# Optimization experiments

Measured on AMD Instinct MI355X. Metric: run time of the kernel, lower is better.

The kernel has to match this reference:

```python
import jax, jax.numpy as jnp
import numpy as np

TOKENS = 1024
IN_W = 512
BLOCK = 256
OUT_W = 512
N_BLOCKS = 64
K = 2


def setup_inputs() -> dict:
    key = jax.random.key(0)
    ks = jax.random.split(key, 8)
    u = lambda k, s: jax.random.uniform(k, s, jnp.float32, -1.0, 1.0)
    return {
        "x": jax.random.normal(ks[0], (TOKENS, IN_W), jnp.float32),
        "noise": jax.random.normal(ks[1], (TOKENS, N_BLOCKS), jnp.float32),
        "w1s": u(ks[2], (N_BLOCKS, IN_W, BLOCK)),
        "b1s": u(ks[3], (N_BLOCKS, BLOCK)),
        "w2s": u(ks[4], (N_BLOCKS, BLOCK, OUT_W)),
        "b2s": u(ks[5], (N_BLOCKS, OUT_W)),
        "mixer": jnp.zeros((IN_W, N_BLOCKS), jnp.float32) + 0.01 * jax.random.normal(ks[6], (IN_W, N_BLOCKS), jnp.float32),
        "noise_controller": jnp.zeros((IN_W, N_BLOCKS), jnp.float32) + 0.01 * jax.random.normal(ks[7], (IN_W, N_BLOCKS), jnp.float32),
        "k": K,
    }


def reference(x, noise, w1s, b1s, w2s, b2s, mixer, noise_controller, k):
    # noisy routing logits: mixer_prod + randn * softplus(noise_prod)
    h_x = x @ mixer + noise * jax.nn.softplus(x @ noise_controller)  # [B, E]
    topk_vals, topk_idx = jax.lax.top_k(h_x, k)                       # [B, K]
    scores = jax.nn.softmax(topk_vals, axis=-1)                       # [B, K]
    # per-token expert weight gather (faithful to index_select semantics)
    gw1 = w1s[topk_idx]  # [B, K, I, H]
    gb1 = b1s[topk_idx]  # [B, K, H]
    gw2 = w2s[topk_idx]  # [B, K, H, O]
    gb2 = b2s[topk_idx]  # [B, K, O]
    v = jax.nn.relu(jnp.einsum('bi,bkih->bkh', x, gw1) + gb1)        # [B, K, H]
    out = jnp.einsum('bkh,bkho->bko', v, gw2) + gb2                   # [B, K, O]
    return jnp.sum(out * scores[..., None], axis=1)                   # [B, O]
```

## Files before the change

kernel.cpp:

```cpp
#include <hip/hip_runtime.h>
#include <math.h>

#define TOKENS    1024
#define IN_W      512
#define BLOCK_H   256
#define OUT_W     512
#define N_EXPERTS 64
#define TOPK      2
#define NSLOTS    (TOKENS * TOPK)
#define LIST_CAP  128
#define T_GRP     12
#define NGRP      4
#define XPAD      520
#define OSPAD     516
#define VPAD      264

__global__ __launch_bounds__(256) void routing_kernel(
    const float* __restrict__ x, const float* __restrict__ noise,
    const float* __restrict__ mixer, const float* __restrict__ noisec,
    float* __restrict__ esc, int* __restrict__ counts, int* __restrict__ lists)
{
    __shared__ float xs[2 * 512];
    __shared__ float pm[2 * 2 * 64];
    __shared__ float pn[2 * 2 * 64];
    const int blk  = blockIdx.x;
    const int tid  = threadIdx.x;
    const int wave = tid >> 6, lane = tid & 63;
    const int tq = wave >> 1;
    const int ih = wave & 1;

    ((float4*)xs)[tid] = ((const float4*)x)[(size_t)blk * 256 + tid];
    __syncthreads();

    float am = 0.f, an = 0.f;
    const float* xp = xs + tq * 512 + ih * 256;
    const float* mp = mixer  + (size_t)(ih * 256) * 64 + lane;
    const float* np = noisec + (size_t)(ih * 256) * 64 + lane;
    #pragma unroll 8
    for (int i = 0; i < 256; ++i) {
        const float xv = xp[i];
        am = fmaf(xv, mp[i * 64], am);
        an = fmaf(xv, np[i * 64], an);
    }
    pm[tq * 128 + ih * 64 + lane] = am;
    pn[tq * 128 + ih * 64 + lane] = an;
    __syncthreads();

    if (tid < 128) {
        const int e = tid & 63, tt = tid >> 6;
        const int t = blk * 2 + tt;
        const float am2 = pm[tt * 128 + e] + pm[tt * 128 + 64 + e];
        const float an2 = pn[tt * 128 + e] + pn[tt * 128 + 64 + e];
        const float sp = fmaxf(an2, 0.f) + log1pf(expf(-fabsf(an2)));
        pm[tt * 128 + e] = am2 + noise[(size_t)t * 64 + e] * sp;
    }
    __syncthreads();

    if (tid < 2) {
        const float* h = pm + tid * 128;
        float b0 = -INFINITY, b1 = -INFINITY;
        int i0 = 0, i1 = 0;
        for (int i = 0; i < N_EXPERTS; ++i) {
            const float v = h[i];
            if (v > b0)      { b1 = b0; i1 = i0; b0 = v; i0 = i; }
            else if (v > b1) { b1 = v; i1 = i; }
        }
        const float z   = expf(b1 - b0);
        const float inv = 1.f / (1.f + z);
        const int t = blk * 2 + tid;
        esc[t * 2 + 0] = inv;
        esc[t * 2 + 1] = z * inv;
        const int p0 = atomicAdd(&counts[i0], 1);
        if (p0 < LIST_CAP) lists[i0 * LIST_CAP + p0] = t * 2 + 0;
        const int p1 = atomicAdd(&counts[i1], 1);
        if (p1 < LIST_CAP) lists[i1 * LIST_CAP + p1] = t * 2 + 1;
    }
}

__global__ __launch_bounds__(1024, 4) void expert_kernel(
    const float* __restrict__ x,
    const float* __restrict__ w1s, const float* __restrict__ b1s,
    const float* __restrict__ w2s, const float* __restrict__ b2s,
    const int* __restrict__ counts, const int* __restrict__ lists,
    const float* __restrict__ esc, float* __restrict__ out)
{
    __shared__ __align__(16) float smem[T_GRP * XPAD];
    __shared__ __align__(16) float vsm[T_GRP * VPAD];
    __shared__ int   slotIds[T_GRP];
    __shared__ float escv[T_GRP];

    const int e  = blockIdx.x;
    const int g  = blockIdx.y;
    const int ne = min(counts[e], LIST_CAP);
    const int tid  = threadIdx.x;
    const int wave = tid >> 6, lane = tid & 63;

    const int cq1  = wave & 3;
    const int tt   = wave >> 2;
    const int c4_1 = cq1 * 16 + (lane & 15);
    const int r1   = lane >> 4;
    const int c4_2 = cq1 * 32 + (lane & 31);
    const int r2   = lane >> 5;
    const int t0   = tt * 3;

    const float4* w1v = (const float4*)(w1s + (size_t)e * IN_W * BLOCK_H);
    const float4* w2v = (const float4*)(w2s + (size_t)e * BLOCK_H * OUT_W);
    const float4* b1v = (const float4*)(b1s + (size_t)e * BLOCK_H);
    const float4* b2v = (const float4*)(b2s + (size_t)e * OUT_W);
    const float4* x4  = (const float4*)x;

    for (int base = g * T_GRP; base < ne; base += NGRP * T_GRP) {
        const int nTok = min(T_GRP, ne - base);
        if (tid < T_GRP) {
            const int s = (tid < nTok) ? lists[e * LIST_CAP + base + tid] : 0;
            slotIds[tid] = s;
            escv[tid]    = esc[s];
        }
        __syncthreads();

        for (int idx = tid; idx < T_GRP * 128; idx += 1024) {
            const int t = idx >> 7, q = idx & 127;
            float4 v = make_float4(0.f, 0.f, 0.f, 0.f);
            if (t < nTok) v = x4[(size_t)(slotIds[t] >> 1) * 128 + q];
            *(float4*)&smem[t * XPAD + q * 4] = v;
        }
        __syncthreads();

        float4 a0 = make_float4(0.f, 0.f, 0.f, 0.f), a1 = a0, a2 = a0;
        {
            const float4* wp = w1v + (size_t)(r1 * 64 + c4_1);
            const float* xb0 = smem + (t0 + 0) * XPAD + r1;
            const float* xb1 = smem + (t0 + 1) * XPAD + r1;
            const float* xb2 = smem + (t0 + 2) * XPAD + r1;
            #pragma unroll 4
            for (int i = 0; i < IN_W; i += 4) {
                const float4 w = wp[(size_t)i * 64];
                const float xv0 = xb0[i], xv1 = xb1[i], xv2 = xb2[i];
                a0.x = fmaf(xv0, w.x, a0.x); a0.y = fmaf(xv0, w.y, a0.y);
                a0.z = fmaf(xv0, w.z, a0.z); a0.w = fmaf(xv0, w.w, a0.w);
                a1.x = fmaf(xv1, w.x, a1.x); a1.y = fmaf(xv1, w.y, a1.y);
                a1.z = fmaf(xv1, w.z, a1.z); a1.w = fmaf(xv1, w.w, a1.w);
                a2.x = fmaf(xv2, w.x, a2.x); a2.y = fmaf(xv2, w.y, a2.y);
                a2.z = fmaf(xv2, w.z, a2.z); a2.w = fmaf(xv2, w.w, a2.w);
            }
        }
        #pragma unroll
        for (int m = 16; m <= 32; m <<= 1) {
            a0.x += __shfl_xor(a0.x, m); a0.y += __shfl_xor(a0.y, m);
            a0.z += __shfl_xor(a0.z, m); a0.w += __shfl_xor(a0.w, m);
            a1.x += __shfl_xor(a1.x, m); a1.y += __shfl_xor(a1.y, m);
            a1.z += __shfl_xor(a1.z, m); a1.w += __shfl_xor(a1.w, m);
            a2.x += __shfl_xor(a2.x, m); a2.y += __shfl_xor(a2.y, m);
            a2.z += __shfl_xor(a2.z, m); a2.w += __shfl_xor(a2.w, m);
        }
        if (lane < 16) {
            const float4 bb = b1v[c4_1];
            float4 r;
            r.x = fmaxf(a0.x + bb.x, 0.f); r.y = fmaxf(a0.y + bb.y, 0.f);
            r.z = fmaxf(a0.z + bb.z, 0.f); r.w = fmaxf(a0.w + bb.w, 0.f);
            *(float4*)&vsm[(t0 + 0) * VPAD + c4_1 * 4] = r;
            r.x = fmaxf(a1.x + bb.x, 0.f); r.y = fmaxf(a1.y + bb.y, 0.f);
            r.z = fmaxf(a1.z + bb.z, 0.f); r.w = fmaxf(a1.w + bb.w, 0.f);
            *(float4*)&vsm[(t0 + 1) * VPAD + c4_1 * 4] = r;
            r.x = fmaxf(a2.x + bb.x, 0.f); r.y = fmaxf(a2.y + bb.y, 0.f);
            r.z = fmaxf(a2.z + bb.z, 0.f); r.w = fmaxf(a2.w + bb.w, 0.f);
            *(float4*)&vsm[(t0 + 2) * VPAD + c4_1 * 4] = r;
        }
        __syncthreads();

        float4 o0 = make_float4(0.f, 0.f, 0.f, 0.f), o1 = o0, o2 = o0;
        {
            const float4* wp2 = w2v + (size_t)(r2 * 128 + c4_2);
            const float* vb0 = vsm + (t0 + 0) * VPAD + r2;
            const float* vb1 = vsm + (t0 + 1) * VPAD + r2;
            const float* vb2 = vsm + (t0 + 2) * VPAD + r2;
            #pragma unroll 4
            for (int h = 0; h < BLOCK_H; h += 2) {
                const float4 w = wp2[(size_t)h * 128];
                const float v0 = vb0[h], v1 = vb1[h], v2 = vb2[h];
                o0.x = fmaf(v0, w.x, o0.x); o0.y = fmaf(v0, w.y, o0.y);
                o0.z = fmaf(v0, w.z, o0.z); o0.w = fmaf(v0, w.w, o0.w);
                o1.x = fmaf(v1, w.x, o1.x); o1.y = fmaf(v1, w.y, o1.y);
                o1.z = fmaf(v1, w.z, o1.z); o1.w = fmaf(v1, w.w, o1.w);
                o2.x = fmaf(v2, w.x, o2.x); o2.y = fmaf(v2, w.y, o2.y);
                o2.z = fmaf(v2, w.z, o2.z); o2.w = fmaf(v2, w.w, o2.w);
            }
        }
        o0.x += __shfl_xor(o0.x, 32); o0.y += __shfl_xor(o0.y, 32);
        o0.z += __shfl_xor(o0.z, 32); o0.w += __shfl_xor(o0.w, 32);
        o1.x += __shfl_xor(o1.x, 32); o1.y += __shfl_xor(o1.y, 32);
        o1.z += __shfl_xor(o1.z, 32); o1.w += __shfl_xor(o1.w, 32);
        o2.x += __shfl_xor(o2.x, 32); o2.y += __shfl_xor(o2.y, 32);
        o2.z += __shfl_xor(o2.z, 32); o2.w += __shfl_xor(o2.w, 32);
        if (lane < 32) {
            *(float4*)&smem[(t0 + 0) * OSPAD + c4_2 * 4] = o0;
            *(float4*)&smem[(t0 + 1) * OSPAD + c4_2 * 4] = o1;
            *(float4*)&smem[(t0 + 2) * OSPAD + c4_2 * 4] = o2;
        }
        __syncthreads();

        for (int idx = tid; idx < T_GRP * 128; idx += 1024) {
            const int t = idx >> 7, q = idx & 127;
            if (t < nTok) {
                const float4 r  = *(const float4*)&smem[t * OSPAD + q * 4];
                const float4 bb = b2v[q];
                const float  sc = escv[t];
                float* o = out + (size_t)(slotIds[t] >> 1) * OUT_W + q * 4;
                atomicAdd(o + 0, (r.x + bb.x) * sc);
                atomicAdd(o + 1, (r.y + bb.y) * sc);
                atomicAdd(o + 2, (r.z + bb.z) * sc);
                atomicAdd(o + 3, (r.w + bb.w) * sc);
            }
        }
        __syncthreads();
    }
}

extern "C" void kernel_launch(void* const* d_in, const int* in_sizes, int n_in,
                              void* d_out, int out_size, void* d_ws, size_t ws_size,
                              hipStream_t stream) {
    const float* x      = (const float*)d_in[0];
    const float* noise  = (const float*)d_in[1];
    const float* w1s    = (const float*)d_in[2];
    const float* b1s    = (const float*)d_in[3];
    const float* w2s    = (const float*)d_in[4];
    const float* b2s    = (const float*)d_in[5];
    const float* mixer  = (const float*)d_in[6];
    const float* noisec = (const float*)d_in[7];
    float* out = (float*)d_out;

    char* ws = (char*)d_ws;
    int*   counts = (int*)ws;                       ws += 256;
    float* esc    = (float*)ws;                     ws += NSLOTS * sizeof(float);
    int*   lists  = (int*)ws;

    hipMemsetAsync(d_out, 0, (size_t)out_size * sizeof(float), stream);
    hipMemsetAsync(counts, 0, 256, stream);

    routing_kernel<<<TOKENS / 2, 256, 0, stream>>>(x, noise, mixer, noisec,
                                                   esc, counts, lists);
    expert_kernel<<<dim3(N_EXPERTS, NGRP), 1024, 0, stream>>>(
        x, w1s, b1s, w2s, b2s, counts, lists, esc, out);
}
```

Baseline: 180.4 us.

## Vectorize LDS activation reads, prefetch weights in registers, retile second GEMM

The first GEMM now gives each lane four consecutive input rows and reads activations from shared memory as float4. Weight rows are double-buffered in registers, so the next 16-row chunk is loaded while the current one is consumed. The second GEMM is retiled so each wave covers 16 output float4 columns for 6 tokens instead of 32 columns for 3 tokens. Each weight load is therefore reused across more tokens, at the cost of more accumulator registers and a two-step shuffle reduction. The larger register footprint under the 1024-thread launch bound could force spills or lower occupancy.

```diff
diff --git a/kernel.cpp b/kernel.cpp
--- a/kernel.cpp
+++ b/kernel.cpp
@@ -95,13 +95,14 @@
     const int tid  = threadIdx.x;
     const int wave = tid >> 6, lane = tid & 63;
 
-    const int cq1  = wave & 3;
-    const int tt   = wave >> 2;
-    const int c4_1 = cq1 * 16 + (lane & 15);
-    const int r1   = lane >> 4;
-    const int c4_2 = cq1 * 32 + (lane & 31);
-    const int r2   = lane >> 5;
-    const int t0   = tt * 3;
+    const int c4 = lane & 15;
+    const int r4 = (lane >> 4) << 2;
+    const int cq1   = wave & 3;
+    const int t0_1  = (wave >> 2) * 3;
+    const int wcol1 = cq1 * 16 + c4;
+    const int co2   = wave & 7;
+    const int t0_2  = (wave >> 3) * 6;
+    const int wcol2 = co2 * 16 + c4;
 
     const float4* w1v = (const float4*)(w1s + (size_t)e * IN_W * BLOCK_H);
     const float4* w2v = (const float4*)(w2s + (size_t)e * BLOCK_H * OUT_W);
@@ -126,76 +127,114 @@
         }
         __syncthreads();
 
-        float4 a0 = make_float4(0.f, 0.f, 0.f, 0.f), a1 = a0, a2 = a0;
         {
-            const float4* wp = w1v + (size_t)(r1 * 64 + c4_1);
-            const float* xb0 = smem + (t0 + 0) * XPAD + r1;
-            const float* xb1 = smem + (t0 + 1) * XPAD + r1;
-            const float* xb2 = smem + (t0 + 2) * XPAD + r1;
-            #pragma unroll 4
-            for (int i = 0; i < IN_W; i += 4) {
-                const float4 w = wp[(size_t)i * 64];
-                const float xv0 = xb0[i], xv1 = xb1[i], xv2 = xb2[i];
-                a0.x = fmaf(xv0, w.x, a0.x); a0.y = fmaf(xv0, w.y, a0.y);
-                a0.z = fmaf(xv0, w.z, a0.z); a0.w = fmaf(xv0, w.w, a0.w);
-                a1.x = fmaf(xv1, w.x, a1.x); a1.y = fmaf(xv1, w.y, a1.y);
-                a1.z = fmaf(xv1, w.z, a1.z); a1.w = fmaf(xv1, w.w, a1.w);
-                a2.x = fmaf(xv2, w.x, a2.x); a2.y = fmaf(xv2, w.y, a2.y);
-                a2.z = fmaf(xv2, w.z, a2.z); a2.w = fmaf(xv2, w.w, a2.w);
-            }
-        }
-        #pragma unroll
-        for (int m = 16; m <= 32; m <<= 1) {
-            a0.x += __shfl_xor(a0.x, m); a0.y += __shfl_xor(a0.y, m);
-            a0.z += __shfl_xor(a0.z, m); a0.w += __shfl_xor(a0.w, m);
-            a1.x += __shfl_xor(a1.x, m); a1.y += __shfl_xor(a1.y, m);
-            a1.z += __shfl_xor(a1.z, m); a1.w += __shfl_xor(a1.w, m);
-            a2.x += __shfl_xor(a2.x, m); a2.y += __shfl_xor(a2.y, m);
-            a2.z += __shfl_xor(a2.z, m); a2.w += __shfl_xor(a2.w, m);
-        }
-        if (lane < 16) {
-            const float4 bb = b1v[c4_1];
-            float4 r;
-            r.x = fmaxf(a0.x + bb.x, 0.f); r.y = fmaxf(a0.y + bb.y, 0.f);
-            r.z = fmaxf(a0.z + bb.z, 0.f); r.w = fmaxf(a0.w + bb.w, 0.f);
-            *(float4*)&vsm[(t0 + 0) * VPAD + c4_1 * 4] = r;
-            r.x = fmaxf(a1.x + bb.x, 0.f); r.y = fmaxf(a1.y + bb.y, 0.f);
-            r.z = fmaxf(a1.z + bb.z, 0.f); r.w = fmaxf(a1.w + bb.w, 0.f);
-            *(float4*)&vsm[(t0 + 1) * VPAD + c4_1 * 4] = r;
-            r.x = fmaxf(a2.x + bb.x, 0.f); r.y = fmaxf(a2.y + bb.y, 0.f);
-            r.z = fmaxf(a2.z + bb.z, 0.f); r.w = fmaxf(a2.w + bb.w, 0.f);
-            *(float4*)&vsm[(t0 + 2) * VPAD + c4_1 * 4] = r;
-        }
-        __syncthreads();
-
-        float4 o0 = make_float4(0.f, 0.f, 0.f, 0.f), o1 = o0, o2 = o0;
+            float4 a0 = make_float4(0.f,0.f,0.f,0.f), a1 = a0, a2 = a0;
+            const float4* wp  = w1v + (size_t)r4 * 64 + wcol1;
+            const float*  xr0 = smem + (t0_1 + 0) * XPAD + r4;
+            const float*  xr1 = smem + (t0_1 + 1) * XPAD + r4;
+            const float*  xr2 = smem + (t0_1 + 2) * XPAD + r4;
+            float4 wb[4], wc[4];
+            #pragma unroll
+            for (int k = 0; k < 4; ++k) wb[k] = wp[(size_t)k * 64];
+            for (int i = 0; i < IN_W; i += 16) {
+                #pragma unroll
+                for (int k = 0; k < 4; ++k) wc[k] = wb[k];
+                if (i + 16 < IN_W) {
+                    #pragma unroll
+                    for (int k = 0; k < 4; ++k)
+                        wb[k] = wp[(size_t)(i + 16 + k) * 64];
+                }
+                const float4 xv0 = *(const float4*)(xr0 + i);
+                const float4 xv1 = *(const float4*)(xr1 + i);
+                const float4 xv2 = *(const float4*)(xr2 + i);
+                const float* f0 = (const float*)&xv0;
+                const float* f1 = (const float*)&xv1;
+                const float* f2 = (const float*)&xv2;
+                #pragma unroll
+                for (int k = 0; k < 4; ++k) {
+                    const float4 w = wc[k];
+                    a0.x = fmaf(f0[k], w.x, a0.x); a0.y = fmaf(f0[k], w.y, a0.y);
+                    a0.z = fmaf(f0[k], w.z, a0.z); a0.w = fmaf(f0[k], w.w, a0.w);
+                    a1.x = fmaf(f1[k], w.x, a1.x); a1.y = fmaf(f1[k], w.y, a1.y);
+                    a1.z = fmaf(f1[k], w.z, a1.z); a1.w = fmaf(f1[k], w.w, a1.w);
+                    a2.x = fmaf(f2[k], w.x, a2.x); a2.y = fmaf(f2[k], w.y, a2.y);
+                    a2.z = fmaf(f2[k], w.z, a2.z); a2.w = fmaf(f2[k], w.w, a2.w);
+                }
+            }
+            #pragma unroll
+            for (int m = 16; m <= 32; m <<= 1) {
+                a0.x += __shfl_xor(a0.x, m); a0.y += __shfl_xor(a0.y, m);
+                a0.z += __shfl_xor(a0.z, m); a0.w += __shfl_xor(a0.w, m);
+                a1.x += __shfl_xor(a1.x, m); a1.y += __shfl_xor(a1.y, m);
+                a1.z += __shfl_xor(a1.z, m); a1.w += __shfl_xor(a1.w, m);
+                a2.x += __shfl_xor(a2.x, m); a2.y += __shfl_xor(a2.y, m);
+                a2.z += __shfl_xor(a2.z, m); a2.w += __shfl_xor(a2.w, m);
+            }
+            if (lane < 16) {
+                const float4 bb = b1v[wcol1];
+                float4 r;
+                r.x = fmaxf(a0.x + bb.x, 0.f); r.y = fmaxf(a0.y + bb.y, 0.f);
+                r.z = fmaxf(a0.z + bb.z, 0.f); r.w = fmaxf(a0.w + bb.w, 0.f);
+                *(float4*)&vsm[(t0_1 + 0) * VPAD + wcol1 * 4] = r;
+                r.x = fmaxf(a1.x + bb.x, 0.f); r.y = fmaxf(a1.y + bb.y, 0.f);
+                r.z = fmaxf(a1.z + bb.z, 0.f); r.w = fmaxf(a1.w + bb.w, 0.f);
+                *(float4*)&vsm[(t0_1 + 1) * VPAD + wcol1 * 4] = r;
+                r.x = fmaxf(a2.x + bb.x, 0.f); r.y = fmaxf(a2.y + bb.y, 0.f);
+                r.z = fmaxf(a2.z + bb.z, 0.f); r.w = fmaxf(a2.w + bb.w, 0.f);
+                *(float4*)&vsm[(t0_1 + 2) * VPAD + wcol1 * 4] = r;
+            }
+        }
+        __syncthreads();
+
         {
-            const float4* wp2 = w2v + (size_t)(r2 * 128 + c4_2);
-            const float* vb0 = vsm + (t0 + 0) * VPAD + r2;
-            const float* vb1 = vsm + (t0 + 1) * VPAD + r2;
-            const float* vb2 = vsm + (t0 + 2) * VPAD + r2;
-            #pragma unroll 4
-            for (int h = 0; h < BLOCK_H; h += 2) {
-                const float4 w = wp2[(size_t)h * 128];
-                const float v0 = vb0[h], v1 = vb1[h], v2 = vb2[h];
-                o0.x = fmaf(v0, w.x, o0.x); o0.y = fmaf(v0, w.y, o0.y);
-                o0.z = fmaf(v0, w.z, o0.z); o0.w = fmaf(v0, w.w, o0.w);
-                o1.x = fmaf(v1, w.x, o1.x); o1.y = fmaf(v1, w.y, o1.y);
-                o1.z = fmaf(v1, w.z, o1.z); o1.w = fmaf(v1, w.w, o1.w);
-                o2.x = fmaf(v2, w.x, o2.x); o2.y = fmaf(v2, w.y, o2.y);
-                o2.z = fmaf(v2, w.z, o2.z); o2.w = fmaf(v2, w.w, o2.w);
-            }
-        }
-        o0.x += __shfl_xor(o0.x, 32); o0.y += __shfl_xor(o0.y, 32);
-        o0.z += __shfl_xor(o0.z, 32); o0.w += __shfl_xor(o0.w, 32);
-        o1.x += __shfl_xor(o1.x, 32); o1.y += __shfl_xor(o1.y, 32);
-        o1.z += __shfl_xor(o1.z, 32); o1.w += __shfl_xor(o1.w, 32);
-        o2.x += __shfl_xor(o2.x, 32); o2.y += __shfl_xor(o2.y, 32);
-        o2.z += __shfl_xor(o2.z, 32); o2.w += __shfl_xor(o2.w, 32);
-        if (lane < 32) {
-            *(float4*)&smem[(t0 + 0) * OSPAD + c4_2 * 4] = o0;
-            *(float4*)&smem[(t0 + 1) * OSPAD + c4_2 * 4] = o1;
-            *(float4*)&smem[(t0 + 2) * OSPAD + c4_2 * 4] = o2;
+            float4 acc[6];
+            #pragma unroll
+            for (int j = 0; j < 6; ++j) acc[j] = make_float4(0.f,0.f,0.f,0.f);
+            const float4* wp2 = w2v + (size_t)r4 * 128 + wcol2;
+            const float*  vr  = vsm + t0_2 * VPAD + r4;
+            float4 wb[4], wc[4];
+            #pragma unroll
+            for (int k = 0; k < 4; ++k) wb[k] = wp2[(size_t)k * 128];
+            for (int h = 0; h < BLOCK_H; h += 16) {
+                #pragma unroll
+                for (int k = 0; k < 4; ++k) wc[k] = wb[k];
+                if (h + 16 < BLOCK_H) {
+                    #pragma unroll
+                    for (int k = 0; k < 4; ++k)
+                        wb[k] = wp2[(size_t)(h + 16 + k) * 128];
+                }
+                float4 vv[6];
+                #pragma unroll
+                for (int j = 0; j < 6; ++j)
+                    vv[j] = *(const float4*)(vr + j * VPAD + h);
+                #pragma unroll
+                for (int k = 0; k < 4; ++k) {
+                    const float4 w = wc[k];
+                    #pragma unroll
+                    for (int j = 0; j < 6; ++j) {
+                        const float s = ((const float*)&vv[j])[k];
+                        acc[j].x = fmaf(s, w.x, acc[j].x);
+                        acc[j].y = fmaf(s, w.y, acc[j].y);
+                        acc[j].z = fmaf(s, w.z, acc[j].z);
+                        acc[j].w = fmaf(s, w.w, acc[j].w);
+                    }
+                }
+            }
+            #pragma unroll
+            for (int m = 16; m <= 32; m <<= 1) {
+                #pragma unroll
+                for (int j = 0; j < 6; ++j) {
+                    acc[j].x += __shfl_xor(acc[j].x, m);
+                    acc[j].y += __shfl_xor(acc[j].y, m);
+                    acc[j].z += __shfl_xor(acc[j].z, m);
+                    acc[j].w += __shfl_xor(acc[j].w, m);
+                }
+            }
+            if (lane < 16) {
+                #pragma unroll
+                for (int j = 0; j < 6; ++j)
+                    *(float4*)&smem[(t0_2 + j) * OSPAD + wcol2 * 4] = acc[j];
+            }
         }
         __syncthreads();
 
```

Result: slower. 185.0 us (+2.6%).
